# Kernel optimization log

Hardware: AMD Instinct MI355X
Metric: run time of the kernel (lower is better)

Reference implementation:

```python
import jax, jax.numpy as jnp
import numpy as np

H, D, BETA = 12, 64, 1.0
EPS = 1e-8


def setup_inputs() -> dict:
    key = jax.random.key(0)
    k1, k2 = jax.random.split(key)
    n, dim = 1024, H * D
    x = jax.random.normal(k1, (n, dim), dtype=jnp.float32)
    mask = jnp.ones((n, n), dtype=bool)
    W_qk = jax.random.normal(k2, (2 * H * D, dim), dtype=jnp.float32) / np.sqrt(dim).astype(np.float32)
    return {"x": x, "mask": mask, "W_qk": W_qk}


def _free_energy_heads(xh, mask, W_qk):
    # xh: (H, n, D) unit-norm token vectors per head -> per-head free energy (H,)
    n = xh.shape[1]
    xf = jnp.transpose(xh, (1, 0, 2)).reshape(n, H * D)      # 'h n d -> n (h d)'
    qk = xf @ W_qk.T                                          # (n, 2*H*D), Linear no-bias
    q, k = jnp.split(qk, 2, axis=-1)
    q = jnp.transpose(q.reshape(n, H, D), (1, 0, 2))          # (H, n, D)
    k = jnp.transpose(k.reshape(n, H, D), (1, 0, 2))
    sim = jnp.einsum('hid,hjd->hij', q, k)                    # (H, n, n)
    sim = jnp.where(mask, sim, jnp.finfo(sim.dtype).min)
    J = jax.scipy.special.logsumexp(sim, axis=-1)             # (H, n)
    # t* = root of quadratic: beta*t^2 + (-0.5 - 2 beta J) t + (beta J^2 + 0.5 J - 0.25 beta |x|^2)
    hn = jnp.sum(xh * xh, axis=-1)                            # (H, n), |x_i|^2
    b = -0.5 - 2.0 * BETA * J
    c = BETA * J ** 2 + 0.5 * J - 0.25 * BETA * hn
    t = (-b + jnp.sqrt(b * b - 4.0 * BETA * c)) / (2.0 * BETA)
    v = t - J                                                 # (H, n)
    inv_v = 1.0 / jnp.clip(v, EPS, jnp.finfo(v.dtype).max)    # safe_reciprocal
    phi = (BETA * jnp.sum(t, axis=-1)
           - 0.5 * jnp.sum(jnp.log(v + EPS), axis=-1)
           + 0.25 * BETA * jnp.sum(hn * inv_v, axis=-1))      # (H,)
    log_Z = -0.5 * n * (1.0 + jnp.log(2.0 * BETA)) + phi
    return -log_Z / BETA                                      # (H,)


def reference(x, mask, W_qk):
    n = x.shape[0]
    xh = jnp.transpose(x.reshape(n, H, D), (1, 0, 2))         # (H, n, D)
    xh = xh / jnp.linalg.norm(xh, axis=-1, keepdims=True)
    jac = jax.jacrev(lambda xs: _free_energy_heads(xs, mask, W_qk))(xh)  # (H, H, n, D)
    diag = jnp.diagonal(jac)                                  # (n, D, H): dF_h/dx_h only
    out = jnp.transpose(diag, (0, 2, 1)).reshape(n, H * D)    # 'n d h -> n (h d)'
    return -out
```

## Files before the change

### kernel.cpp

```cpp
#include <hip/hip_runtime.h>
#include <hip/hip_cooperative_groups.h>
#include <cstdint>

namespace cg = cooperative_groups;

#define NTOK 1024
#define NH   12
#define HD   64
#define DIM  768
#define QKD  1536

static constexpr float C2G = 0.61803398874989485f;

typedef __bf16 bf16x8 __attribute__((ext_vector_type(8)));
typedef __bf16 bf16x4 __attribute__((ext_vector_type(4)));
typedef float  f32x4  __attribute__((ext_vector_type(4)));

#define MFMA16(a, b, c) __builtin_amdgcn_mfma_f32_16x16x32_bf16((a), (b), (c), 0, 0, 0)

#define FRAG(S, outer, ks) (*(const bf16x8*)&S[(outer) + (l & 15)][(ks) * 32 + (l >> 4) * 8])

__global__ __launch_bounds__(256) void fused_k(
    const float* __restrict__ x, const float* __restrict__ W,
    float* __restrict__ xf, __bf16* __restrict__ xhb,
    __bf16* __restrict__ Wb, __bf16* __restrict__ WT,
    __bf16* __restrict__ qkb, __bf16* __restrict__ qkT,
    float* __restrict__ part_k, float* __restrict__ part_q,
    float* __restrict__ part_z, float* __restrict__ out) {
  cg::grid_group grid = cg::this_grid();
  __shared__ __align__(16) __bf16 T[6][64][72];
  __shared__ float Zs[64];
  const int b = blockIdx.x, t = threadIdx.x, l = t & 63, w = t >> 6;
  const int R = (w >> 1) * 32, Cc = (w & 1) * 32;
  const int srow = t >> 2, scol = (t & 3) * 16;

  {
#pragma unroll
    for (int rep = 0; rep < 8; ++rep) {
      int gid = b * 32 + rep * 4 + w;
      int i = gid / NH, h = gid - i * NH;
      size_t idx = (size_t)i * DIM + h * HD + l;
      float v = x[idx];
      float ss = v * v;
#pragma unroll
      for (int m = 1; m < 64; m <<= 1) ss += __shfl_xor(ss, m);
      float r = v * rsqrtf(ss);
      xf[idx] = r;
      xhb[idx] = (__bf16)r;
    }
#pragma unroll
    for (int rep = 0; rep < 3; ++rep) {
      int tg = (rep * 384 + b) * 256 + t;
      float4 v = ((const float4*)W)[tg];
      bf16x4 o;
      o[0] = (__bf16)v.x; o[1] = (__bf16)v.y; o[2] = (__bf16)v.z; o[3] = (__bf16)v.w;
      *(bf16x4*)(Wb + (size_t)tg * 4) = o;
    }
    if (b < 24) {
      float (*Ws)[65] = (float(*)[65])T;
      int h = b % NH, p = b / NH;
      int rowbase = p * DIM + h * HD;
#pragma unroll
      for (int rr = 0; rr < 16; ++rr) {
        int row = rr * 4 + (t >> 6), col = t & 63;
        Ws[row][col] = W[(size_t)(rowbase + row) * DIM + h * HD + col];
      }
      __syncthreads();
      __bf16* dst = WT + ((size_t)p * NH + h) * HD * HD;
#pragma unroll
      for (int rr = 0; rr < 16; ++rr) {
        int dlt = rr * 4 + (t >> 6), d = t & 63;
        dst[dlt * HD + d] = (__bf16)Ws[d][dlt];
      }
    }
  }
  __threadfence();
  grid.sync();

  {
    int m0 = (b & 15) * 64, n0 = (b >> 4) * 64;
    uint4 aA = *(const uint4*)(xhb + (size_t)(m0 + srow) * DIM + scol);
    uint4 aB = *(const uint4*)(xhb + (size_t)(m0 + srow) * DIM + scol + 8);
    uint4 bA = *(const uint4*)(Wb  + (size_t)(n0 + srow) * DIM + scol);
    uint4 bB = *(const uint4*)(Wb  + (size_t)(n0 + srow) * DIM + scol + 8);
    f32x4 acc[2][2] = {};
    for (int kt = 0; kt < 12; ++kt) {
      int buf = kt & 1;
      *(uint4*)&T[buf][srow][scol]         = aA;
      *(uint4*)&T[buf][srow][scol + 8]     = aB;
      *(uint4*)&T[2 + buf][srow][scol]     = bA;
      *(uint4*)&T[2 + buf][srow][scol + 8] = bB;
      if (kt < 11) {
        int k0 = (kt + 1) * 64;
        aA = *(const uint4*)(xhb + (size_t)(m0 + srow) * DIM + k0 + scol);
        aB = *(const uint4*)(xhb + (size_t)(m0 + srow) * DIM + k0 + scol + 8);
        bA = *(const uint4*)(Wb  + (size_t)(n0 + srow) * DIM + k0 + scol);
        bB = *(const uint4*)(Wb  + (size_t)(n0 + srow) * DIM + k0 + scol + 8);
      }
      __syncthreads();
#pragma unroll
      for (int ks = 0; ks < 2; ++ks) {
        bf16x8 af[2], bf[2];
#pragma unroll
        for (int mf = 0; mf < 2; ++mf) af[mf] = FRAG(T[buf], R + mf * 16, ks);
#pragma unroll
        for (int nf = 0; nf < 2; ++nf) bf[nf] = FRAG(T[2 + buf], Cc + nf * 16, ks);
#pragma unroll
        for (int mf = 0; mf < 2; ++mf)
#pragma unroll
          for (int nf = 0; nf < 2; ++nf) acc[mf][nf] = MFMA16(af[mf], bf[nf], acc[mf][nf]);
      }
    }
#pragma unroll
    for (int mf = 0; mf < 2; ++mf)
#pragma unroll
      for (int nf = 0; nf < 2; ++nf) {
        int rowb = m0 + R + mf * 16 + (l >> 4) * 4;
        int col  = n0 + Cc + nf * 16 + (l & 15);
        bf16x4 o4;
#pragma unroll
        for (int r = 0; r < 4; ++r) {
          __bf16 v = (__bf16)acc[mf][nf][r];
          o4[r] = v;
          qkb[(size_t)(rowb + r) * QKD + col] = v;
        }
        *(bf16x4*)(qkT + (size_t)col * NTOK + rowb) = o4;
      }
  }
  __threadfence();
  grid.sync();

  {
    int h = b >> 5, rem = b & 31;
    int i0 = (rem >> 1) * 64;
    int jt0 = (rem & 1) * 8;
    const __bf16* kbase  = qkb + DIM + h * HD;
    const __bf16* ktbase = qkT + (size_t)(DIM + h * HD + srow) * NTOK;
    *(uint4*)&T[0][srow][scol]     = *(const uint4*)(qkb + (size_t)(i0 + srow) * QKD + h * HD + scol);
    *(uint4*)&T[0][srow][scol + 8] = *(const uint4*)(qkb + (size_t)(i0 + srow) * QKD + h * HD + scol + 8);
    if (t < 64) Zs[t] = 0.f;
    uint4 kA = *(const uint4*)(kbase + (size_t)(jt0 * 64 + srow) * QKD + scol);
    uint4 kB = *(const uint4*)(kbase + (size_t)(jt0 * 64 + srow) * QKD + scol + 8);
    uint4 tA = *(const uint4*)(ktbase + jt0 * 64 + scol);
    uint4 tB = *(const uint4*)(ktbase + jt0 * 64 + scol + 8);
    f32x4 facc[2][2] = {};
    float zacc[8] = {0.f, 0.f, 0.f, 0.f, 0.f, 0.f, 0.f, 0.f};
    for (int jt = jt0; jt < jt0 + 8; ++jt) {
      int buf = jt & 1;
      *(uint4*)&T[1 + buf][srow][scol]     = kA;
      *(uint4*)&T[1 + buf][srow][scol + 8] = kB;
      *(uint4*)&T[3 + buf][srow][scol]     = tA;
      *(uint4*)&T[3 + buf][srow][scol + 8] = tB;
      if (jt < jt0 + 7) {
        int j0 = (jt + 1) * 64;
        kA = *(const uint4*)(kbase + (size_t)(j0 + srow) * QKD + scol);
        kB = *(const uint4*)(kbase + (size_t)(j0 + srow) * QKD + scol + 8);
        tA = *(const uint4*)(ktbase + j0 + scol);
        tB = *(const uint4*)(ktbase + j0 + scol + 8);
      }
      __syncthreads();
      f32x4 sacc[2][2] = {};
#pragma unroll
      for (int ks = 0; ks < 2; ++ks) {
        bf16x8 af[2], bf[2];
#pragma unroll
        for (int mf = 0; mf < 2; ++mf) af[mf] = FRAG(T[0], R + mf * 16, ks);
#pragma unroll
        for (int nf = 0; nf < 2; ++nf) bf[nf] = FRAG(T[1 + buf], Cc + nf * 16, ks);
#pragma unroll
        for (int mf = 0; mf < 2; ++mf)
#pragma unroll
          for (int nf = 0; nf < 2; ++nf) sacc[mf][nf] = MFMA16(af[mf], bf[nf], sacc[mf][nf]);
      }
#pragma unroll
      for (int mf = 0; mf < 2; ++mf)
#pragma unroll
        for (int r = 0; r < 4; ++r) {
          float e0 = __expf(sacc[mf][0][r]);
          float e1 = __expf(sacc[mf][1][r]);
          zacc[mf * 4 + r] += e0 + e1;
          int row = R + mf * 16 + (l >> 4) * 4 + r;
          T[5][row][Cc + (l & 15)]      = (__bf16)e0;
          T[5][row][Cc + 16 + (l & 15)] = (__bf16)e1;
        }
      __syncthreads();
#pragma unroll
      for (int ks = 0; ks < 2; ++ks) {
        bf16x8 af[2], bf[2];
#pragma unroll
        for (int mf = 0; mf < 2; ++mf) af[mf] = FRAG(T[5], R + mf * 16, ks);
#pragma unroll
        for (int nf = 0; nf < 2; ++nf) bf[nf] = FRAG(T[3 + buf], Cc + nf * 16, ks);
#pragma unroll
        for (int mf = 0; mf < 2; ++mf)
#pragma unroll
          for (int nf = 0; nf < 2; ++nf) facc[mf][nf] = MFMA16(af[mf], bf[nf], facc[mf][nf]);
      }
    }
    float* pk = part_k + (size_t)b * 4096;
#pragma unroll
    for (int mf = 0; mf < 2; ++mf)
#pragma unroll
      for (int nf = 0; nf < 2; ++nf)
#pragma unroll
        for (int r = 0; r < 4; ++r) {
          int row = R + mf * 16 + (l >> 4) * 4 + r;
          int col = Cc + nf * 16 + (l & 15);
          pk[row * 64 + col] = facc[mf][nf][r];
        }
#pragma unroll
    for (int zi = 0; zi < 8; ++zi) {
      float z = zacc[zi];
      z += __shfl_xor(z, 1); z += __shfl_xor(z, 2);
      z += __shfl_xor(z, 4); z += __shfl_xor(z, 8);
      if ((l & 15) == 0) {
        int row = R + (zi >> 2) * 16 + (l >> 4) * 4 + (zi & 3);
        atomicAdd(&Zs[row], z);
      }
    }
    __syncthreads();
    if (t < 64) part_z[(size_t)b * 64 + t] = Zs[t];
  }
  __threadfence();
  grid.sync();

  {
    int h = b >> 5, rem = b & 31;
    int j0 = (rem >> 1) * 64;
    int it0 = (rem & 1) * 8;
    const __bf16* qbase  = qkb + h * HD;
    const __bf16* qtbase = qkT + (size_t)(h * HD + srow) * NTOK;
    const float*  pz     = part_z + (size_t)h * 2048;
    *(uint4*)&T[0][srow][scol]     = *(const uint4*)(qkb + (size_t)(j0 + srow) * QKD + DIM + h * HD + scol);
    *(uint4*)&T[0][srow][scol + 8] = *(const uint4*)(qkb + (size_t)(j0 + srow) * QKD + DIM + h * HD + scol + 8);
    uint4 qA = *(const uint4*)(qbase + (size_t)(it0 * 64 + srow) * QKD + scol);
    uint4 qB = *(const uint4*)(qbase + (size_t)(it0 * 64 + srow) * QKD + scol + 8);
    uint4 tA = *(const uint4*)(qtbase + it0 * 64 + scol);
    uint4 tB = *(const uint4*)(qtbase + it0 * 64 + scol + 8);
    f32x4 facc[2][2] = {};
    for (int it = it0; it < it0 + 8; ++it) {
      int buf = it & 1;
      *(uint4*)&T[1 + buf][srow][scol]     = qA;
      *(uint4*)&T[1 + buf][srow][scol + 8] = qB;
      *(uint4*)&T[3 + buf][srow][scol]     = tA;
      *(uint4*)&T[3 + buf][srow][scol + 8] = tB;
      if (it < it0 + 7) {
        int i0 = (it + 1) * 64;
        qA = *(const uint4*)(qbase + (size_t)(i0 + srow) * QKD + scol);
        qB = *(const uint4*)(qbase + (size_t)(i0 + srow) * QKD + scol + 8);
        tA = *(const uint4*)(qtbase + i0 + scol);
        tB = *(const uint4*)(qtbase + i0 + scol + 8);
      }
      __syncthreads();
      f32x4 sacc[2][2] = {};
#pragma unroll
      for (int ks = 0; ks < 2; ++ks) {
        bf16x8 af[2], bf[2];
#pragma unroll
        for (int mf = 0; mf < 2; ++mf) af[mf] = FRAG(T[0], R + mf * 16, ks);
#pragma unroll
        for (int nf = 0; nf < 2; ++nf) bf[nf] = FRAG(T[1 + buf], Cc + nf * 16, ks);
#pragma unroll
        for (int mf = 0; mf < 2; ++mf)
#pragma unroll
          for (int nf = 0; nf < 2; ++nf) sacc[mf][nf] = MFMA16(af[mf], bf[nf], sacc[mf][nf]);
      }
      float iz0 = 1.0f / (pz[it * 128 + Cc + (l & 15)]      + pz[it * 128 + 64 + Cc + (l & 15)]);
      float iz1 = 1.0f / (pz[it * 128 + Cc + 16 + (l & 15)] + pz[it * 128 + 64 + Cc + 16 + (l & 15)]);
#pragma unroll
      for (int mf = 0; mf < 2; ++mf)
#pragma unroll
        for (int r = 0; r < 4; ++r) {
          float e0 = __expf(sacc[mf][0][r]) * iz0;
          float e1 = __expf(sacc[mf][1][r]) * iz1;
          int row = R + mf * 16 + (l >> 4) * 4 + r;
          T[5][row][Cc + (l & 15)]      = (__bf16)e0;
          T[5][row][Cc + 16 + (l & 15)] = (__bf16)e1;
        }
      __syncthreads();
#pragma unroll
      for (int ks = 0; ks < 2; ++ks) {
        bf16x8 af[2], bf[2];
#pragma unroll
        for (int mf = 0; mf < 2; ++mf) af[mf] = FRAG(T[5], R + mf * 16, ks);
#pragma unroll
        for (int nf = 0; nf < 2; ++nf) bf[nf] = FRAG(T[3 + buf], Cc + nf * 16, ks);
#pragma unroll
        for (int mf = 0; mf < 2; ++mf)
#pragma unroll
          for (int nf = 0; nf < 2; ++nf) facc[mf][nf] = MFMA16(af[mf], bf[nf], facc[mf][nf]);
      }
    }
    float* pq = part_q + (size_t)b * 4096;
#pragma unroll
    for (int mf = 0; mf < 2; ++mf)
#pragma unroll
      for (int nf = 0; nf < 2; ++nf)
#pragma unroll
        for (int r = 0; r < 4; ++r) {
          int row = R + mf * 16 + (l >> 4) * 4 + r;
          int col = Cc + nf * 16 + (l & 15);
          pq[row * 64 + col] = facc[mf][nf][r];
        }
  }
  __threadfence();
  grid.sync();

  if (b < 192) {
    int h = b >> 4, jidx = b & 15, j0 = jidx * 64;
    const float* pk = part_k + ((size_t)(h * 32 + jidx * 2)) * 4096;
    const float* pq = part_q + ((size_t)(h * 32 + jidx * 2)) * 4096;
    const float* pzr = part_z + ((size_t)(h * 32 + jidx * 2)) * 64;
#pragma unroll
    for (int mf = 0; mf < 2; ++mf)
#pragma unroll
      for (int r = 0; r < 4; ++r) {
        int row = R + mf * 16 + (l >> 4) * 4 + r;
        float iz = 1.0f / (pzr[row] + pzr[64 + row]);
#pragma unroll
        for (int nf = 0; nf < 2; ++nf) {
          int col = Cc + nf * 16 + (l & 15);
          int off = row * 64 + col;
          T[0][row][col] = (__bf16)((pk[off] + pk[4096 + off]) * iz);
          T[1][row][col] = (__bf16)(pq[off] + pq[4096 + off]);
        }
      }
    const __bf16* wq = WT + (size_t)h * HD * HD;
    const __bf16* wk = WT + ((size_t)NH + h) * HD * HD;
    *(uint4*)&T[2][srow][scol]     = *(const uint4*)(wq + (size_t)srow * HD + scol);
    *(uint4*)&T[2][srow][scol + 8] = *(const uint4*)(wq + (size_t)srow * HD + scol + 8);
    *(uint4*)&T[3][srow][scol]     = *(const uint4*)(wk + (size_t)srow * HD + scol);
    *(uint4*)&T[3][srow][scol + 8] = *(const uint4*)(wk + (size_t)srow * HD + scol + 8);
    __syncthreads();
    f32x4 acc[2][2] = {};
#pragma unroll
    for (int ks = 0; ks < 2; ++ks) {
      bf16x8 af[2], bf[2];
#pragma unroll
      for (int mf = 0; mf < 2; ++mf) af[mf] = FRAG(T[0], R + mf * 16, ks);
#pragma unroll
      for (int nf = 0; nf < 2; ++nf) bf[nf] = FRAG(T[2], Cc + nf * 16, ks);
#pragma unroll
      for (int mf = 0; mf < 2; ++mf)
#pragma unroll
        for (int nf = 0; nf < 2; ++nf) acc[mf][nf] = MFMA16(af[mf], bf[nf], acc[mf][nf]);
    }
#pragma unroll
    for (int ks = 0; ks < 2; ++ks) {
      bf16x8 af[2], bf[2];
#pragma unroll
      for (int mf = 0; mf < 2; ++mf) af[mf] = FRAG(T[1], R + mf * 16, ks);
#pragma unroll
      for (int nf = 0; nf < 2; ++nf) bf[nf] = FRAG(T[3], Cc + nf * 16, ks);
#pragma unroll
      for (int mf = 0; mf < 2; ++mf)
#pragma unroll
        for (int nf = 0; nf < 2; ++nf) acc[mf][nf] = MFMA16(af[mf], bf[nf], acc[mf][nf]);
    }
#pragma unroll
    for (int mf = 0; mf < 2; ++mf)
#pragma unroll
      for (int nf = 0; nf < 2; ++nf)
#pragma unroll
        for (int r = 0; r < 4; ++r) {
          int row = j0 + R + mf * 16 + (l >> 4) * 4 + r;
          int col = h * HD + Cc + nf * 16 + (l & 15);
          size_t idx = (size_t)row * DIM + col;
          out[idx] = acc[mf][nf][r] + C2G * xf[idx];
        }
  }
}

__global__ __launch_bounds__(256) void prep_k(const float* __restrict__ x,
                                              const float* __restrict__ W,
                                              float* __restrict__ xf,
                                              __bf16* __restrict__ xhb,
                                              __bf16* __restrict__ Wb,
                                              __bf16* __restrict__ WT,
                                              float* __restrict__ Zg) {
  __shared__ float Ws[64][65];
  int b = blockIdx.x, t = threadIdx.x;
  if (b < 3072) {
    int gid  = b * 4 + (t >> 6);
    int lane = t & 63;
    int i = gid / NH, h = gid - i * NH;
    size_t idx = (size_t)i * DIM + h * HD + lane;
    float v = x[idx];
    float ss = v * v;
#pragma unroll
    for (int m = 1; m < 64; m <<= 1) ss += __shfl_xor(ss, m);
    float r = v * rsqrtf(ss);
    xf[idx] = r;
    xhb[idx] = (__bf16)r;
  } else if (b < 4224) {
    int tg = (b - 3072) * 256 + t;
    float4 v = ((const float4*)W)[tg];
    bf16x4 o;
    o[0] = (__bf16)v.x; o[1] = (__bf16)v.y; o[2] = (__bf16)v.z; o[3] = (__bf16)v.w;
    *(bf16x4*)(Wb + (size_t)tg * 4) = o;
  } else if (b < 4248) {
    int bb = b - 4224;
    int h = bb % NH, p = bb / NH;
    int rowbase = p * DIM + h * HD;
#pragma unroll
    for (int rr = 0; rr < 16; ++rr) {
      int row = rr * 4 + (t >> 6), col = t & 63;
      Ws[row][col] = W[(size_t)(rowbase + row) * DIM + h * HD + col];
    }
    __syncthreads();
    __bf16* dst = WT + ((size_t)p * NH + h) * HD * HD;
#pragma unroll
    for (int rr = 0; rr < 16; ++rr) {
      int dlt = rr * 4 + (t >> 6), d = t & 63;
      dst[dlt * HD + d] = (__bf16)Ws[d][dlt];
    }
  } else {
    int zz = b - 4248;
    ((float4*)Zg)[zz * 256 + t] = make_float4(0.f, 0.f, 0.f, 0.f);
  }
}

__global__ __launch_bounds__(256) void gemm_dual_k(const __bf16* __restrict__ A,
                                                   const __bf16* __restrict__ Bt,
                                                   __bf16* __restrict__ qkb,
                                                   __bf16* __restrict__ qkT) {
  __shared__ __align__(16) __bf16 As[2][64][72], Bs[2][64][72];
  int m0 = blockIdx.x * 64, n0 = blockIdx.y * 64;
  int t = threadIdx.x, l = t & 63, w = t >> 6;
  int R = (w >> 1) * 32, Cc = (w & 1) * 32;
  int srow = t >> 2, scol = (t & 3) * 16;
  uint4 aA = *(const uint4*)(A  + (size_t)(m0 + srow) * DIM + scol);
  uint4 aB = *(const uint4*)(A  + (size_t)(m0 + srow) * DIM + scol + 8);
  uint4 bA = *(const uint4*)(Bt + (size_t)(n0 + srow) * DIM + scol);
  uint4 bB = *(const uint4*)(Bt + (size_t)(n0 + srow) * DIM + scol + 8);
  f32x4 acc[2][2] = {};
  for (int kt = 0; kt < 12; ++kt) {
    int buf = kt & 1;
    *(uint4*)&As[buf][srow][scol]     = aA;
    *(uint4*)&As[buf][srow][scol + 8] = aB;
    *(uint4*)&Bs[buf][srow][scol]     = bA;
    *(uint4*)&Bs[buf][srow][scol + 8] = bB;
    if (kt < 11) {
      int k0 = (kt + 1) * 64;
      aA = *(const uint4*)(A  + (size_t)(m0 + srow) * DIM + k0 + scol);
      aB = *(const uint4*)(A  + (size_t)(m0 + srow) * DIM + k0 + scol + 8);
      bA = *(const uint4*)(Bt + (size_t)(n0 + srow) * DIM + k0 + scol);
      bB = *(const uint4*)(Bt + (size_t)(n0 + srow) * DIM + k0 + scol + 8);
    }
    __syncthreads();
#pragma unroll
    for (int ks = 0; ks < 2; ++ks) {
      bf16x8 af[2], bf[2];
#pragma unroll
      for (int mf = 0; mf < 2; ++mf) af[mf] = FRAG(As[buf], R + mf * 16, ks);
#pragma unroll
      for (int nf = 0; nf < 2; ++nf) bf[nf] = FRAG(Bs[buf], Cc + nf * 16, ks);
#pragma unroll
      for (int mf = 0; mf < 2; ++mf)
#pragma unroll
        for (int nf = 0; nf < 2; ++nf) acc[mf][nf] = MFMA16(af[mf], bf[nf], acc[mf][nf]);
    }
  }
#pragma unroll
  for (int mf = 0; mf < 2; ++mf)
#pragma unroll
    for (int nf = 0; nf < 2; ++nf) {
      int rowb = m0 + R + mf * 16 + (l >> 4) * 4;
      int col  = n0 + Cc + nf * 16 + (l & 15);
      bf16x4 o4;
#pragma unroll
      for (int r = 0; r < 4; ++r) {
        __bf16 v = (__bf16)acc[mf][nf][r];
        o4[r] = v;
        qkb[(size_t)(rowb + r) * QKD + col] = v;
      }
      *(bf16x4*)(qkT + (size_t)col * NTOK + rowb) = o4;
    }
}

__global__ __launch_bounds__(256) void kbarp_k(const __bf16* __restrict__ qkb,
                                               const __bf16* __restrict__ qkT,
                                               float* __restrict__ part_k,
                                               float* __restrict__ Zg) {
  __shared__ __align__(16) __bf16 Qs[64][72], Ks[2][64][72], KTs[2][64][72], Es[64][72];
  int u = blockIdx.x;
  int h = u >> 5, rem = u & 31;
  int i0 = (rem >> 1) * 64;
  int jt0 = (rem & 1) * 8;
  int t = threadIdx.x, l = t & 63, w = t >> 6;
  int R = (w >> 1) * 32, Cc = (w & 1) * 32;
  int srow = t >> 2, scol = (t & 3) * 16;
  const __bf16* kbase  = qkb + DIM + h * HD;
  const __bf16* ktbase = qkT + (size_t)(DIM + h * HD + srow) * NTOK;
  *(uint4*)&Qs[srow][scol]     = *(const uint4*)(qkb + (size_t)(i0 + srow) * QKD + h * HD + scol);
  *(uint4*)&Qs[srow][scol + 8] = *(const uint4*)(qkb + (size_t)(i0 + srow) * QKD + h * HD + scol + 8);
  uint4 kA = *(const uint4*)(kbase + (size_t)(jt0 * 64 + srow) * QKD + scol);
  uint4 kB = *(const uint4*)(kbase + (size_t)(jt0 * 64 + srow) * QKD + scol + 8);
  uint4 tA = *(const uint4*)(ktbase + jt0 * 64 + scol);
  uint4 tB = *(const uint4*)(ktbase + jt0 * 64 + scol + 8);
  f32x4 facc[2][2] = {};
  float zacc[8] = {0.f, 0.f, 0.f, 0.f, 0.f, 0.f, 0.f, 0.f};
  for (int jt = jt0; jt < jt0 + 8; ++jt) {
    int buf = jt & 1;
    *(uint4*)&Ks[buf][srow][scol]      = kA;
    *(uint4*)&Ks[buf][srow][scol + 8]  = kB;
    *(uint4*)&KTs[buf][srow][scol]     = tA;
    *(uint4*)&KTs[buf][srow][scol + 8] = tB;
    if (jt < jt0 + 7) {
      int j0 = (jt + 1) * 64;
      kA = *(const uint4*)(kbase + (size_t)(j0 + srow) * QKD + scol);
      kB = *(const uint4*)(kbase + (size_t)(j0 + srow) * QKD + scol + 8);
      tA = *(const uint4*)(ktbase + j0 + scol);
      tB = *(const uint4*)(ktbase + j0 + scol + 8);
    }
    __syncthreads();
    f32x4 sacc[2][2] = {};
#pragma unroll
    for (int ks = 0; ks < 2; ++ks) {
      bf16x8 af[2], bf[2];
#pragma unroll
      for (int mf = 0; mf < 2; ++mf) af[mf] = FRAG(Qs, R + mf * 16, ks);
#pragma unroll
      for (int nf = 0; nf < 2; ++nf) bf[nf] = FRAG(Ks[buf], Cc + nf * 16, ks);
#pragma unroll
      for (int mf = 0; mf < 2; ++mf)
#pragma unroll
        for (int nf = 0; nf < 2; ++nf) sacc[mf][nf] = MFMA16(af[mf], bf[nf], sacc[mf][nf]);
    }
#pragma unroll
    for (int mf = 0; mf < 2; ++mf)
#pragma unroll
      for (int r = 0; r < 4; ++r) {
        float e0 = __expf(sacc[mf][0][r]);
        float e1 = __expf(sacc[mf][1][r]);
        zacc[mf * 4 + r] += e0 + e1;
        int row = R + mf * 16 + (l >> 4) * 4 + r;
        Es[row][Cc + (l & 15)]      = (__bf16)e0;
        Es[row][Cc + 16 + (l & 15)] = (__bf16)e1;
      }
    __syncthreads();
#pragma unroll
    for (int ks = 0; ks < 2; ++ks) {
      bf16x8 af[2], bf[2];
#pragma unroll
      for (int mf = 0; mf < 2; ++mf) af[mf] = FRAG(Es, R + mf * 16, ks);
#pragma unroll
      for (int nf = 0; nf < 2; ++nf) bf[nf] = FRAG(KTs[buf], Cc + nf * 16, ks);
#pragma unroll
      for (int mf = 0; mf < 2; ++mf)
#pragma unroll
        for (int nf = 0; nf < 2; ++nf) facc[mf][nf] = MFMA16(af[mf], bf[nf], facc[mf][nf]);
    }
  }
  float* pk = part_k + (size_t)u * 4096;
#pragma unroll
  for (int mf = 0; mf < 2; ++mf)
#pragma unroll
    for (int nf = 0; nf < 2; ++nf)
#pragma unroll
      for (int r = 0; r < 4; ++r) {
        int row = R + mf * 16 + (l >> 4) * 4 + r;
        int col = Cc + nf * 16 + (l & 15);
        pk[row * 64 + col] = facc[mf][nf][r];
      }
#pragma unroll
  for (int zi = 0; zi < 8; ++zi) {
    float z = zacc[zi];
    z += __shfl_xor(z, 1); z += __shfl_xor(z, 2);
    z += __shfl_xor(z, 4); z += __shfl_xor(z, 8);
    if ((l & 15) == 0) {
      int row = R + (zi >> 2) * 16 + (l >> 4) * 4 + (zi & 3);
      atomicAdd(&Zg[(size_t)h * NTOK + i0 + row], z);
    }
  }
}

__global__ __launch_bounds__(256) void qbarp_k(const __bf16* __restrict__ qkb,
                                               const __bf16* __restrict__ qkT,
                                               const float* __restrict__ Zg,
                                               float* __restrict__ part_q) {
  __shared__ __align__(16) __bf16 Ks[64][72], Qs[2][64][72], QTs[2][64][72], Es[64][72];
  int u = blockIdx.x;
  int h = u >> 5, rem = u & 31;
  int j0 = (rem >> 1) * 64;
  int it0 = (rem & 1) * 8;
  int t = threadIdx.x, l = t & 63, w = t >> 6;
  int R = (w >> 1) * 32, Cc = (w & 1) * 32;
  int srow = t >> 2, scol = (t & 3) * 16;
  const __bf16* qbase  = qkb + h * HD;
  const __bf16* qtbase = qkT + (size_t)(h * HD + srow) * NTOK;
  const float*  zb     = Zg + (size_t)h * NTOK;
  *(uint4*)&Ks[srow][scol]     = *(const uint4*)(qkb + (size_t)(j0 + srow) * QKD + DIM + h * HD + scol);
  *(uint4*)&Ks[srow][scol + 8] = *(const uint4*)(qkb + (size_t)(j0 + srow) * QKD + DIM + h * HD + scol + 8);
  uint4 qA = *(const uint4*)(qbase + (size_t)(it0 * 64 + srow) * QKD + scol);
  uint4 qB = *(const uint4*)(qbase + (size_t)(it0 * 64 + srow) * QKD + scol + 8);
  uint4 tA = *(const uint4*)(qtbase + it0 * 64 + scol);
  uint4 tB = *(const uint4*)(qtbase + it0 * 64 + scol + 8);
  f32x4 facc[2][2] = {};
  for (int it = it0; it < it0 + 8; ++it) {
    int buf = it & 1;
    *(uint4*)&Qs[buf][srow][scol]      = qA;
    *(uint4*)&Qs[buf][srow][scol + 8]  = qB;
    *(uint4*)&QTs[buf][srow][scol]     = tA;
    *(uint4*)&QTs[buf][srow][scol + 8] = tB;
    if (it < it0 + 7) {
      int i0 = (it + 1) * 64;
      qA = *(const uint4*)(qbase + (size_t)(i0 + srow) * QKD + scol);
      qB = *(const uint4*)(qbase + (size_t)(i0 + srow) * QKD + scol + 8);
      tA = *(const uint4*)(qtbase + i0 + scol);
      tB = *(const uint4*)(qtbase + i0 + scol + 8);
    }
    __syncthreads();
    f32x4 sacc[2][2] = {};
#pragma unroll
    for (int ks = 0; ks < 2; ++ks) {
      bf16x8 af[2], bf[2];
#pragma unroll
      for (int mf = 0; mf < 2; ++mf) af[mf] = FRAG(Ks, R + mf * 16, ks);
#pragma unroll
      for (int nf = 0; nf < 2; ++nf) bf[nf] = FRAG(Qs[buf], Cc + nf * 16, ks);
#pragma unroll
      for (int mf = 0; mf < 2; ++mf)
#pragma unroll
        for (int nf = 0; nf < 2; ++nf) sacc[mf][nf] = MFMA16(af[mf], bf[nf], sacc[mf][nf]);
    }
    float iz0 = 1.0f / zb[it * 64 + Cc + (l & 15)];
    float iz1 = 1.0f / zb[it * 64 + Cc + 16 + (l & 15)];
#pragma unroll
    for (int mf = 0; mf < 2; ++mf)
#pragma unroll
      for (int r = 0; r < 4; ++r) {
        float e0 = __expf(sacc[mf][0][r]) * iz0;
        float e1 = __expf(sacc[mf][1][r]) * iz1;
        int row = R + mf * 16 + (l >> 4) * 4 + r;
        Es[row][Cc + (l & 15)]      = (__bf16)e0;
        Es[row][Cc + 16 + (l & 15)] = (__bf16)e1;
      }
    __syncthreads();
#pragma unroll
    for (int ks = 0; ks < 2; ++ks) {
      bf16x8 af[2], bf[2];
#pragma unroll
      for (int mf = 0; mf < 2; ++mf) af[mf] = FRAG(Es, R + mf * 16, ks);
#pragma unroll
      for (int nf = 0; nf < 2; ++nf) bf[nf] = FRAG(QTs[buf], Cc + nf * 16, ks);
#pragma unroll
      for (int mf = 0; mf < 2; ++mf)
#pragma unroll
        for (int nf = 0; nf < 2; ++nf) facc[mf][nf] = MFMA16(af[mf], bf[nf], facc[mf][nf]);
    }
  }
  float* pq = part_q + (size_t)u * 4096;
#pragma unroll
  for (int mf = 0; mf < 2; ++mf)
#pragma unroll
    for (int nf = 0; nf < 2; ++nf)
#pragma unroll
      for (int r = 0; r < 4; ++r) {
        int row = R + mf * 16 + (l >> 4) * 4 + r;
        int col = Cc + nf * 16 + (l & 15);
        pq[row * 64 + col] = facc[mf][nf][r];
      }
}

__global__ __launch_bounds__(256) void final2_k(const float* __restrict__ part_k,
                                                const float* __restrict__ part_q,
                                                const float* __restrict__ Zg,
                                                const __bf16* __restrict__ WT,
                                                const float* __restrict__ xf,
                                                float* __restrict__ out) {
  __shared__ __align__(16) __bf16 Ka[64][72], Qa[64][72], WqS[64][72], WkS[64][72];
  int u = blockIdx.x;
  int h = u >> 4, jidx = u & 15, j0 = jidx * 64;
  int t = threadIdx.x, l = t & 63, w = t >> 6;
  int R = (w >> 1) * 32, Cc = (w & 1) * 32;
  int srow = t >> 2, scol = (t & 3) * 16;
  const float* pk = part_k + ((size_t)(h * 32 + jidx * 2)) * 4096;
  const float* pq = part_q + ((size_t)(h * 32 + jidx * 2)) * 4096;
#pragma unroll
  for (int mf = 0; mf < 2; ++mf)
#pragma unroll
    for (int r = 0; r < 4; ++r) {
      int row = R + mf * 16 + (l >> 4) * 4 + r;
      float iz = 1.0f / Zg[(size_t)h * NTOK + j0 + row];
#pragma unroll
      for (int nf = 0; nf < 2; ++nf) {
        int col = Cc + nf * 16 + (l & 15);
        int off = row * 64 + col;
        Ka[row][col] = (__bf16)((pk[off] + pk[4096 + off]) * iz);
        Qa[row][col] = (__bf16)(pq[off] + pq[4096 + off]);
      }
    }
  const __bf16* wq = WT + (size_t)h * HD * HD;
  const __bf16* wk = WT + ((size_t)NH + h) * HD * HD;
  *(uint4*)&WqS[srow][scol]     = *(const uint4*)(wq + (size_t)srow * HD + scol);
  *(uint4*)&WqS[srow][scol + 8] = *(const uint4*)(wq + (size_t)srow * HD + scol + 8);
  *(uint4*)&WkS[srow][scol]     = *(const uint4*)(wk + (size_t)srow * HD + scol);
  *(uint4*)&WkS[srow][scol + 8] = *(const uint4*)(wk + (size_t)srow * HD + scol + 8);
  __syncthreads();
  f32x4 acc[2][2] = {};
#pragma unroll
  for (int ks = 0; ks < 2; ++ks) {
    bf16x8 af[2], bf[2];
#pragma unroll
    for (int mf = 0; mf < 2; ++mf) af[mf] = FRAG(Ka, R + mf * 16, ks);
#pragma unroll
    for (int nf = 0; nf < 2; ++nf) bf[nf] = FRAG(WqS, Cc + nf * 16, ks);
#pragma unroll
    for (int mf = 0; mf < 2; ++mf)
#pragma unroll
      for (int nf = 0; nf < 2; ++nf) acc[mf][nf] = MFMA16(af[mf], bf[nf], acc[mf][nf]);
  }
#pragma unroll
  for (int ks = 0; ks < 2; ++ks) {
    bf16x8 af[2], bf[2];
#pragma unroll
    for (int mf = 0; mf < 2; ++mf) af[mf] = FRAG(Qa, R + mf * 16, ks);
#pragma unroll
    for (int nf = 0; nf < 2; ++nf) bf[nf] = FRAG(WkS, Cc + nf * 16, ks);
#pragma unroll
    for (int mf = 0; mf < 2; ++mf)
#pragma unroll
      for (int nf = 0; nf < 2; ++nf) acc[mf][nf] = MFMA16(af[mf], bf[nf], acc[mf][nf]);
  }
#pragma unroll
  for (int mf = 0; mf < 2; ++mf)
#pragma unroll
    for (int nf = 0; nf < 2; ++nf)
#pragma unroll
      for (int r = 0; r < 4; ++r) {
        int row = j0 + R + mf * 16 + (l >> 4) * 4 + r;
        int col = h * HD + Cc + nf * 16 + (l & 15);
        size_t idx = (size_t)row * DIM + col;
        out[idx] = acc[mf][nf][r] + C2G * xf[idx];
      }
}

extern "C" void kernel_launch(void* const* d_in, const int* in_sizes, int n_in,
                              void* d_out, int out_size, void* d_ws, size_t ws_size,
                              hipStream_t stream) {
  const float* x = (const float*)d_in[0];
  const float* W = (const float*)d_in[2];
  float* out = (float*)d_out;

  float* wsf = (float*)d_ws;
  size_t off = 0;
  float* xf     = wsf + off; off += (size_t)NTOK * DIM;
  float* Zg     = wsf + off; off += (size_t)NH * NTOK;
  float* part_k = wsf + off; off += (size_t)384 * 4096;
  float* part_q = wsf + off; off += (size_t)384 * 4096;
  float* part_z = wsf + off; off += (size_t)384 * 64;
  __bf16* wsb = (__bf16*)(wsf + off);
  size_t boff = 0;
  __bf16* xhb = wsb + boff; boff += (size_t)NTOK * DIM;
  __bf16* Wb  = wsb + boff; boff += (size_t)QKD * DIM;
  __bf16* WT  = wsb + boff; boff += (size_t)2 * NH * HD * HD;
  __bf16* qkb = wsb + boff; boff += (size_t)NTOK * QKD;
  __bf16* qkT = wsb + boff; boff += (size_t)QKD * NTOK;

  int maxb = 0;
  hipOccupancyMaxActiveBlocksPerMultiprocessor(&maxb, fused_k, 256, 0);
  int dev = 0, ncu = 0;
  hipGetDevice(&dev);
  hipDeviceGetAttribute(&ncu, hipDeviceAttributeMultiprocessorCount, dev);
  bool coop = (maxb > 0 && ncu > 0 && (long)maxb * ncu >= 384);

  if (coop) {
    void* args[] = {(void*)&x, (void*)&W, (void*)&xf, (void*)&xhb, (void*)&Wb,
                    (void*)&WT, (void*)&qkb, (void*)&qkT, (void*)&part_k,
                    (void*)&part_q, (void*)&part_z, (void*)&out};
    hipLaunchCooperativeKernel(fused_k, dim3(384), dim3(256), args, 0, stream);
  } else {
    prep_k<<<dim3(4260), dim3(256), 0, stream>>>(x, W, xf, xhb, Wb, WT, Zg);
    gemm_dual_k<<<dim3(16, 24), dim3(256), 0, stream>>>(xhb, Wb, qkb, qkT);
    kbarp_k<<<dim3(384), dim3(256), 0, stream>>>(qkb, qkT, part_k, Zg);
    qbarp_k<<<dim3(384), dim3(256), 0, stream>>>(qkb, qkT, Zg, part_q);
    final2_k<<<dim3(192), dim3(256), 0, stream>>>(part_k, part_q, Zg, WT, xf, out);
  }
}
```

Measured before the change: 50.27 us.

## Fuse normalization and bf16 conversion into QK GEMM and merge final phases

Normalization of x and bf16 conversion of x and W now happen inside the QK GEMM's tile loads, removing the prep phase and one grid-wide barrier. The q-side reduction now covers all 16 i-tiles in one block and feeds its result straight into the final projection, removing the part_q round trip and another grid barrier. GEMM output is staged through LDS so qkb and qkT are written with coalesced 16-byte stores. In exchange, the q phase runs on only 192 blocks with twice the serial loop length, and the fp32 inputs are re-read by every block that tiles them.

```diff
diff --git a/kernel.cpp b/kernel.cpp
--- a/kernel.cpp
+++ b/kernel.cpp
@@ -20,13 +20,19 @@
 
 #define FRAG(S, outer, ks) (*(const bf16x8*)&S[(outer) + (l & 15)][(ks) * 32 + (l >> 4) * 8])
 
+__device__ __forceinline__ bf16x4 cvt4(float4 v, float s) {
+  bf16x4 o;
+  o[0] = (__bf16)(v.x * s); o[1] = (__bf16)(v.y * s);
+  o[2] = (__bf16)(v.z * s); o[3] = (__bf16)(v.w * s);
+  return o;
+}
+
 __global__ __launch_bounds__(256) void fused_k(
     const float* __restrict__ x, const float* __restrict__ W,
-    float* __restrict__ xf, __bf16* __restrict__ xhb,
-    __bf16* __restrict__ Wb, __bf16* __restrict__ WT,
+    float* __restrict__ xf, __bf16* __restrict__ WT,
     __bf16* __restrict__ qkb, __bf16* __restrict__ qkT,
-    float* __restrict__ part_k, float* __restrict__ part_q,
-    float* __restrict__ part_z, float* __restrict__ out) {
+    float* __restrict__ part_k, float* __restrict__ part_z,
+    float* __restrict__ out) {
   cg::grid_group grid = cg::this_grid();
   __shared__ __align__(16) __bf16 T[6][64][72];
   __shared__ float Zs[64];
@@ -35,27 +41,9 @@
   const int srow = t >> 2, scol = (t & 3) * 16;
 
   {
-#pragma unroll
-    for (int rep = 0; rep < 8; ++rep) {
-      int gid = b * 32 + rep * 4 + w;
-      int i = gid / NH, h = gid - i * NH;
-      size_t idx = (size_t)i * DIM + h * HD + l;
-      float v = x[idx];
-      float ss = v * v;
-#pragma unroll
-      for (int m = 1; m < 64; m <<= 1) ss += __shfl_xor(ss, m);
-      float r = v * rsqrtf(ss);
-      xf[idx] = r;
-      xhb[idx] = (__bf16)r;
-    }
-#pragma unroll
-    for (int rep = 0; rep < 3; ++rep) {
-      int tg = (rep * 384 + b) * 256 + t;
-      float4 v = ((const float4*)W)[tg];
-      bf16x4 o;
-      o[0] = (__bf16)v.x; o[1] = (__bf16)v.y; o[2] = (__bf16)v.z; o[3] = (__bf16)v.w;
-      *(bf16x4*)(Wb + (size_t)tg * 4) = o;
-    }
+    int m0 = (b & 15) * 64, n0 = (b >> 4) * 64;
+    bool wxf = (b >> 4) == 0;
+
     if (b < 24) {
       float (*Ws)[65] = (float(*)[65])T;
       int h = b % NH, p = b / NH;
@@ -72,30 +60,42 @@
         int dlt = rr * 4 + (t >> 6), d = t & 63;
         dst[dlt * HD + d] = (__bf16)Ws[d][dlt];
       }
-    }
-  }
-  __threadfence();
-  grid.sync();
-
-  {
-    int m0 = (b & 15) * 64, n0 = (b >> 4) * 64;
-    uint4 aA = *(const uint4*)(xhb + (size_t)(m0 + srow) * DIM + scol);
-    uint4 aB = *(const uint4*)(xhb + (size_t)(m0 + srow) * DIM + scol + 8);
-    uint4 bA = *(const uint4*)(Wb  + (size_t)(n0 + srow) * DIM + scol);
-    uint4 bB = *(const uint4*)(Wb  + (size_t)(n0 + srow) * DIM + scol + 8);
+      __syncthreads();
+    }
+
+    const float* xrow = x + (size_t)(m0 + srow) * DIM + scol;
+    const float* wrow = W + (size_t)(n0 + srow) * DIM + scol;
+    float4 a4[4], b4[4];
+#pragma unroll
+    for (int q = 0; q < 4; ++q) {
+      a4[q] = *(const float4*)(xrow + q * 4);
+      b4[q] = *(const float4*)(wrow + q * 4);
+    }
     f32x4 acc[2][2] = {};
     for (int kt = 0; kt < 12; ++kt) {
       int buf = kt & 1;
-      *(uint4*)&T[buf][srow][scol]         = aA;
-      *(uint4*)&T[buf][srow][scol + 8]     = aB;
-      *(uint4*)&T[2 + buf][srow][scol]     = bA;
-      *(uint4*)&T[2 + buf][srow][scol + 8] = bB;
+      float ss = 0.f;
+#pragma unroll
+      for (int q = 0; q < 4; ++q)
+        ss += a4[q].x * a4[q].x + a4[q].y * a4[q].y + a4[q].z * a4[q].z + a4[q].w * a4[q].w;
+      ss += __shfl_xor(ss, 1);
+      ss += __shfl_xor(ss, 2);
+      float inv = rsqrtf(ss);
+#pragma unroll
+      for (int q = 0; q < 4; ++q) {
+        *(bf16x4*)&T[buf][srow][scol + q * 4]     = cvt4(a4[q], inv);
+        *(bf16x4*)&T[2 + buf][srow][scol + q * 4] = cvt4(b4[q], 1.0f);
+        if (wxf) {
+          float4 av = make_float4(a4[q].x * inv, a4[q].y * inv, a4[q].z * inv, a4[q].w * inv);
+          *(float4*)(xf + (size_t)(m0 + srow) * DIM + kt * 64 + scol + q * 4) = av;
+        }
+      }
       if (kt < 11) {
-        int k0 = (kt + 1) * 64;
-        aA = *(const uint4*)(xhb + (size_t)(m0 + srow) * DIM + k0 + scol);
-        aB = *(const uint4*)(xhb + (size_t)(m0 + srow) * DIM + k0 + scol + 8);
-        bA = *(const uint4*)(Wb  + (size_t)(n0 + srow) * DIM + k0 + scol);
-        bB = *(const uint4*)(Wb  + (size_t)(n0 + srow) * DIM + k0 + scol + 8);
+#pragma unroll
+        for (int q = 0; q < 4; ++q) {
+          a4[q] = *(const float4*)(xrow + (kt + 1) * 64 + q * 4);
+          b4[q] = *(const float4*)(wrow + (kt + 1) * 64 + q * 4);
+        }
       }
       __syncthreads();
 #pragma unroll
@@ -114,18 +114,20 @@
 #pragma unroll
     for (int mf = 0; mf < 2; ++mf)
 #pragma unroll
-      for (int nf = 0; nf < 2; ++nf) {
-        int rowb = m0 + R + mf * 16 + (l >> 4) * 4;
-        int col  = n0 + Cc + nf * 16 + (l & 15);
-        bf16x4 o4;
+      for (int nf = 0; nf < 2; ++nf)
 #pragma unroll
         for (int r = 0; r < 4; ++r) {
+          int row = R + mf * 16 + (l >> 4) * 4 + r;
+          int col = Cc + nf * 16 + (l & 15);
           __bf16 v = (__bf16)acc[mf][nf][r];
-          o4[r] = v;
-          qkb[(size_t)(rowb + r) * QKD + col] = v;
+          T[4][row][col] = v;
+          T[5][col][row] = v;
         }
-        *(bf16x4*)(qkT + (size_t)col * NTOK + rowb) = o4;
-      }
+    __syncthreads();
+    *(uint4*)(qkb + (size_t)(m0 + srow) * QKD + n0 + scol)     = *(const uint4*)&T[4][srow][scol];
+    *(uint4*)(qkb + (size_t)(m0 + srow) * QKD + n0 + scol + 8) = *(const uint4*)&T[4][srow][scol + 8];
+    *(uint4*)(qkT + (size_t)(n0 + srow) * NTOK + m0 + scol)     = *(const uint4*)&T[5][srow][scol];
+    *(uint4*)(qkT + (size_t)(n0 + srow) * NTOK + m0 + scol + 8) = *(const uint4*)&T[5][srow][scol + 8];
   }
   __threadfence();
   grid.sync();
@@ -224,27 +226,25 @@
   __threadfence();
   grid.sync();
 
-  {
-    int h = b >> 5, rem = b & 31;
-    int j0 = (rem >> 1) * 64;
-    int it0 = (rem & 1) * 8;
+  if (b < 192) {
+    int h = b >> 4, jidx = b & 15, j0 = jidx * 64;
     const __bf16* qbase  = qkb + h * HD;
     const __bf16* qtbase = qkT + (size_t)(h * HD + srow) * NTOK;
     const float*  pz     = part_z + (size_t)h * 2048;
     *(uint4*)&T[0][srow][scol]     = *(const uint4*)(qkb + (size_t)(j0 + srow) * QKD + DIM + h * HD + scol);
     *(uint4*)&T[0][srow][scol + 8] = *(const uint4*)(qkb + (size_t)(j0 + srow) * QKD + DIM + h * HD + scol + 8);
-    uint4 qA = *(const uint4*)(qbase + (size_t)(it0 * 64 + srow) * QKD + scol);
-    uint4 qB = *(const uint4*)(qbase + (size_t)(it0 * 64 + srow) * QKD + scol + 8);
-    uint4 tA = *(const uint4*)(qtbase + it0 * 64 + scol);
-    uint4 tB = *(const uint4*)(qtbase + it0 * 64 + scol + 8);
+    uint4 qA = *(const uint4*)(qbase + (size_t)srow * QKD + scol);
+    uint4 qB = *(const uint4*)(qbase + (size_t)srow * QKD + scol + 8);
+    uint4 tA = *(const uint4*)(qtbase + scol);
+    uint4 tB = *(const uint4*)(qtbase + scol + 8);
     f32x4 facc[2][2] = {};
-    for (int it = it0; it < it0 + 8; ++it) {
+    for (int it = 0; it < 16; ++it) {
       int buf = it & 1;
       *(uint4*)&T[1 + buf][srow][scol]     = qA;
       *(uint4*)&T[1 + buf][srow][scol + 8] = qB;
       *(uint4*)&T[3 + buf][srow][scol]     = tA;
       *(uint4*)&T[3 + buf][srow][scol + 8] = tB;
-      if (it < it0 + 7) {
+      if (it < 15) {
         int i0 = (it + 1) * 64;
         qA = *(const uint4*)(qbase + (size_t)(i0 + srow) * QKD + scol);
         qB = *(const uint4*)(qbase + (size_t)(i0 + srow) * QKD + scol + 8);
@@ -291,26 +291,9 @@
           for (int nf = 0; nf < 2; ++nf) facc[mf][nf] = MFMA16(af[mf], bf[nf], facc[mf][nf]);
       }
     }
-    float* pq = part_q + (size_t)b * 4096;
-#pragma unroll
-    for (int mf = 0; mf < 2; ++mf)
-#pragma unroll
-      for (int nf = 0; nf < 2; ++nf)
-#pragma unroll
-        for (int r = 0; r < 4; ++r) {
-          int row = R + mf * 16 + (l >> 4) * 4 + r;
-          int col = Cc + nf * 16 + (l & 15);
-          pq[row * 64 + col] = facc[mf][nf][r];
-        }
-  }
-  __threadfence();
-  grid.sync();
-
-  if (b < 192) {
-    int h = b >> 4, jidx = b & 15, j0 = jidx * 64;
-    const float* pk = part_k + ((size_t)(h * 32 + jidx * 2)) * 4096;
-    const float* pq = part_q + ((size_t)(h * 32 + jidx * 2)) * 4096;
-    const float* pzr = part_z + ((size_t)(h * 32 + jidx * 2)) * 64;
+    __syncthreads();
+    const float* pk  = part_k + (size_t)(h * 32 + jidx * 2) * 4096;
+    const float* pzr = part_z + (size_t)(h * 32 + jidx * 2) * 64;
 #pragma unroll
     for (int mf = 0; mf < 2; ++mf)
 #pragma unroll
@@ -322,7 +305,7 @@
           int col = Cc + nf * 16 + (l & 15);
           int off = row * 64 + col;
           T[0][row][col] = (__bf16)((pk[off] + pk[4096 + off]) * iz);
-          T[1][row][col] = (__bf16)(pq[off] + pq[4096 + off]);
+          T[1][row][col] = (__bf16)facc[mf][nf][r];
         }
       }
     const __bf16* wq = WT + (size_t)h * HD * HD;
@@ -332,7 +315,7 @@
     *(uint4*)&T[3][srow][scol]     = *(const uint4*)(wk + (size_t)srow * HD + scol);
     *(uint4*)&T[3][srow][scol + 8] = *(const uint4*)(wk + (size_t)srow * HD + scol + 8);
     __syncthreads();
-    f32x4 acc[2][2] = {};
+    f32x4 acc2[2][2] = {};
 #pragma unroll
     for (int ks = 0; ks < 2; ++ks) {
       bf16x8 af[2], bf[2];
@@ -343,7 +326,7 @@
 #pragma unroll
       for (int mf = 0; mf < 2; ++mf)
 #pragma unroll
-        for (int nf = 0; nf < 2; ++nf) acc[mf][nf] = MFMA16(af[mf], bf[nf], acc[mf][nf]);
+        for (int nf = 0; nf < 2; ++nf) acc2[mf][nf] = MFMA16(af[mf], bf[nf], acc2[mf][nf]);
     }
 #pragma unroll
     for (int ks = 0; ks < 2; ++ks) {
@@ -355,7 +338,7 @@
 #pragma unroll
       for (int mf = 0; mf < 2; ++mf)
 #pragma unroll
-        for (int nf = 0; nf < 2; ++nf) acc[mf][nf] = MFMA16(af[mf], bf[nf], acc[mf][nf]);
+        for (int nf = 0; nf < 2; ++nf) acc2[mf][nf] = MFMA16(af[mf], bf[nf], acc2[mf][nf]);
     }
 #pragma unroll
     for (int mf = 0; mf < 2; ++mf)
@@ -366,7 +349,7 @@
           int row = j0 + R + mf * 16 + (l >> 4) * 4 + r;
           int col = h * HD + Cc + nf * 16 + (l & 15);
           size_t idx = (size_t)row * DIM + col;
-          out[idx] = acc[mf][nf][r] + C2G * xf[idx];
+          out[idx] = acc2[mf][nf][r] + C2G * xf[idx];
         }
   }
 }
@@ -766,9 +749,9 @@
   bool coop = (maxb > 0 && ncu > 0 && (long)maxb * ncu >= 384);
 
   if (coop) {
-    void* args[] = {(void*)&x, (void*)&W, (void*)&xf, (void*)&xhb, (void*)&Wb,
-                    (void*)&WT, (void*)&qkb, (void*)&qkT, (void*)&part_k,
-                    (void*)&part_q, (void*)&part_z, (void*)&out};
+    void* args[] = {(void*)&x, (void*)&W, (void*)&xf, (void*)&WT,
+                    (void*)&qkb, (void*)&qkT, (void*)&part_k, (void*)&part_z,
+                    (void*)&out};
     hipLaunchCooperativeKernel(fused_k, dim3(384), dim3(256), args, 0, stream);
   } else {
     prep_k<<<dim3(4260), dim3(256), 0, stream>>>(x, W, xf, xhb, Wb, WT, Zg);
```

After: 50.54 us. No clear change (+0.5%).
